# Kernel optimization log

Measured on AMD Instinct MI355X. Metric: run time of the kernel, lower is better.

Reference implementation:

```python
import jax, jax.numpy as jnp
import numpy as np


def setup_inputs() -> dict:
    key = jax.random.key(0)
    ks = jax.random.split(key, 5)
    B, C, H, W = 4, 256, 64, 64
    Cq = C // 8
    x = jax.random.normal(ks[0], (B, C, H, W), dtype=jnp.float32)
    Wq = jax.random.normal(ks[1], (Cq, C), dtype=jnp.float32) * (1.0 / np.sqrt(C))
    Wk = jax.random.normal(ks[2], (Cq, C), dtype=jnp.float32) * (1.0 / np.sqrt(C))
    Wv = jax.random.normal(ks[3], (C, C), dtype=jnp.float32) * (1.0 / np.sqrt(C))
    bq = jnp.zeros((Cq,), dtype=jnp.float32)
    bk = jnp.zeros((Cq,), dtype=jnp.float32)
    bv = jnp.zeros((C,), dtype=jnp.float32)
    gamma = jnp.ones((1,), dtype=jnp.float32)
    return {"x": x, "Wq": Wq, "bq": bq, "Wk": Wk, "bk": bk, "Wv": Wv, "bv": bv, "gamma": gamma}


def reference(x, Wq, bq, Wk, bk, Wv, bv, gamma):
    B, C, H, W = x.shape
    N = H * W
    xf = x.reshape(B, C, N)                      # (B, C, N)
    # 1x1 convs == per-pixel linear projections over channels
    q = jnp.einsum('dc,bcn->bdn', Wq, xf) + bq[None, :, None]   # (B, C/8, N)
    k = jnp.einsum('dc,bcn->bdn', Wk, xf) + bk[None, :, None]   # (B, C/8, N)
    v = jnp.einsum('dc,bcn->bdn', Wv, xf) + bv[None, :, None]   # (B, C,   N)
    # attention: note original has NO 1/sqrt(d) scaling
    scores = jnp.einsum('bdn,bdm->bnm', q, k)     # (B, N, N)
    attn = jax.nn.softmax(scores, axis=-1)
    out = jnp.einsum('bnm,bdm->bnd', attn, v)     # (B, N, C)
    out = out.transpose(0, 2, 1).reshape(B, C, H, W)
    return gamma * out + x
```

## Files before the change

kernel.cpp:

```cpp
#include <hip/hip_runtime.h>

#define BATCH 4
#define CH    256
#define DQ    32
#define NPIX  4096
#define LOG2E 1.44269504088896340736f

typedef unsigned short u16;
typedef unsigned int   u32;
typedef __attribute__((ext_vector_type(8))) short short8;
typedef __attribute__((ext_vector_type(16))) float f32x16;

__device__ __align__(16) u16 g_wbf[10 * 2 * 8192];
__device__ float g_bias[10 * 32];

__device__ __forceinline__ float b2f(u32 u) {
  union { u32 i; float f; } v; v.i = (u & 0xffffu) << 16; return v.f;
}
__device__ __forceinline__ u16 f2b(float f) {
  union { float f; u32 i; } v; v.f = f;
  u32 x = v.i; x += 0x7fffu + ((x >> 16) & 1u);
  return (u16)(x >> 16);
}
__device__ __forceinline__ float fexp2(float x) {
#if __has_builtin(__builtin_amdgcn_exp2f)
  return __builtin_amdgcn_exp2f(x);
#else
  return __expf(x * 0.69314718055994530942f);
#endif
}
__device__ __forceinline__ u32 cvtpk_bf16(float a, float b) {
  u32 r;
  asm("v_cvt_pk_bf16_f32 %0, %1, %2" : "=v"(r) : "v"(a), "v"(b));
  return r;
}

__device__ __forceinline__ void half_swap(u32 a0, u32 a1, u32 b0, u32 b1,
                                          int hl, uint4& o) {
#if __has_builtin(__builtin_amdgcn_permlane32_swap)
  const auto r0 = __builtin_amdgcn_permlane32_swap((int)a0, (int)b0, false, false);
  const auto r1 = __builtin_amdgcn_permlane32_swap((int)a1, (int)b1, false, false);
  o.x = (u32)r0[0]; o.y = (u32)r1[0]; o.z = (u32)r0[1]; o.w = (u32)r1[1];
#else
  const u32 s0 = hl ? a0 : b0;
  const u32 s1 = hl ? a1 : b1;
  const u32 r0 = (u32)__shfl_xor((int)s0, 32);
  const u32 r1 = (u32)__shfl_xor((int)s1, 32);
  o.x = hl ? r0 : a0; o.y = hl ? r1 : a1;
  o.z = hl ? b0 : r0; o.w = hl ? b1 : r1;
#endif
}

__global__ __launch_bounds__(256) void xprep(
    const float* __restrict__ x, u16* __restrict__ xt_hi, u16* __restrict__ xt_lo,
    const float* __restrict__ Wq, const float* __restrict__ bq,
    const float* __restrict__ Wk, const float* __restrict__ bk,
    const float* __restrict__ Wv, const float* __restrict__ bv)
{
  const int t = threadIdx.x;

  if (blockIdx.z == BATCH) {
    if (blockIdx.y != 0 || blockIdx.x >= 10) return;
    const int jt = blockIdx.x;
    const float* Wsrc; const float* bsrc; int jrow0; float scale = 1.f;
    if (jt == 0)      { Wsrc = Wq; bsrc = bq; jrow0 = 0; scale = LOG2E; }
    else if (jt == 1) { Wsrc = Wk; bsrc = bk; jrow0 = 0; }
    else              { Wsrc = Wv; bsrc = bv; jrow0 = (jt - 2) * 32; }
    u16* wdst = g_wbf + (size_t)jt * 16384;
    for (int i = 0; i < 32; ++i) {
      const int flat = i * 256 + t;
      const int j = flat >> 8, e = flat & 255;
      const float v = Wsrc[(size_t)(jrow0 + j) * CH + e] * scale;
      const u16 hi = f2b(v);
      const u16 lo = f2b(v - b2f(hi));
      const int idx = (((e >> 4) * 2 + ((e >> 3) & 1)) * 32 + j) * 8 + (e & 7);
      wdst[idx] = hi; wdst[8192 + idx] = lo;
    }
    if (t < 32) g_bias[jt * 32 + t] = bsrc[jrow0 + t] * scale;
    return;
  }

  const int nt = blockIdx.x, kb4 = blockIdx.y * 4, b = blockIdx.z;
  const int n0 = nt * 128, c0 = blockIdx.y * 64;
  __shared__ u32 xls[64][129];

  const int tn = t & 127, cp = t >> 7;
  for (int i = 0; i < 32; ++i) {
    const int c = cp + 2 * i;
    const float v = x[((size_t)b * CH + c0 + c) * NPIX + n0 + tn];
    const u16 h = f2b(v);
    const u16 l = f2b(v - b2f(h));
    xls[c][tn] = (u32)h | ((u32)l << 16);
  }
  __syncthreads();

  for (int rep = 0; rep < 4; ++rep) {
    const int id = t + 256 * rep;
    const int kkhl = id >> 7, n = id & 127;
    union { short8 s; uint4 u; } vh, vl;
    #pragma unroll
    for (int j = 0; j < 8; ++j) {
      const u32 p = xls[kkhl * 8 + j][n];
      vh.s[j] = (short)(p & 0xffffu);
      vl.s[j] = (short)(p >> 16);
    }
    const size_t o = ((((size_t)(b * 32 + nt) * 16 + kb4 + (kkhl >> 1)) * 2
                       + (kkhl & 1)) * 128 + n) * 8;
    *(uint4*)(xt_hi + o) = vh.u;
    *(uint4*)(xt_lo + o) = vl.u;
  }
}

__global__ __launch_bounds__(256, 4) void proj(
    const u16* __restrict__ xt_hi, const u16* __restrict__ xt_lo,
    u16* __restrict__ q_t, u16* __restrict__ k_t, u16* __restrict__ v_swz)
{
  const int L = blockIdx.x;
  const int xcd = L & 7, s = L >> 3;
  const int jt = s >> 4;
  const int pair = xcd * 16 + (s & 15);
  const int nt = pair >> 2, b = pair & 3;

  const int t = threadIdx.x;
  const int w = t >> 6, lane = t & 63, hl = lane >> 5, l31 = lane & 31;
  const int nb = w * 32 + l31, n = nt * 128 + nb;

  const u16* __restrict__ wb = g_wbf + (size_t)jt * 16384;
  const size_t xtile = (size_t)(b * 32 + nt) * 16 * 2 * 128 * 8;
  const u16* __restrict__ xh = xt_hi + xtile;
  const u16* __restrict__ xl = xt_lo + xtile;

  f32x16 acc1, acc2;
  #pragma unroll
  for (int r = 0; r < 16; ++r) { acc1[r] = 0.f; acc2[r] = 0.f; }

  #pragma unroll
  for (int kk = 0; kk < 16; ++kk) {
    const int aoff = ((kk * 2 + hl) * 32 + l31) * 8;
    const short8 wah = *(const short8*)(wb + aoff);
    const short8 wal = *(const short8*)(wb + 8192 + aoff);
    const int boff = ((kk * 2 + hl) * 128 + nb) * 8;
    const short8 xbh = *(const short8*)(xh + boff);
    const short8 xbl = *(const short8*)(xl + boff);
    acc1 = __builtin_amdgcn_mfma_f32_32x32x16_bf16(wah, xbh, acc1, 0, 0, 0);
    acc2 = __builtin_amdgcn_mfma_f32_32x32x16_bf16(wah, xbl, acc2, 0, 0, 0);
    acc2 = __builtin_amdgcn_mfma_f32_32x32x16_bf16(wal, xbh, acc2, 0, 0, 0);
  }

  f32x16 accv;
  #pragma unroll
  for (int r = 0; r < 16; ++r)
    accv[r] = acc1[r] + acc2[r]
            + g_bias[jt * 32 + (r & 3) + 8 * (r >> 2) + 4 * hl];

  if (jt <= 1) {
    u16* dst = (jt == 0) ? q_t : k_t;
    #pragma unroll
    for (int r2 = 0; r2 < 4; ++r2) {
      uint2 pk;
      pk.x = (u32)f2b(accv[4 * r2 + 0]) | ((u32)f2b(accv[4 * r2 + 1]) << 16);
      pk.y = (u32)f2b(accv[4 * r2 + 2]) | ((u32)f2b(accv[4 * r2 + 3]) << 16);
      *(uint2*)(dst + ((size_t)b * NPIX + n) * DQ + 4 * hl + 8 * r2) = pk;
    }
  } else {
    const int mc = nt * 4 + w;
    const int kc = (l31 >> 4) & 1, h3 = (l31 >> 3) & 1, j8 = l31 & 7;
    u16* dst = v_swz + (((((size_t)b * 128 + mc) * 8 + (jt - 2)) * 2 + kc) * 2 + h3) * 256 + j8;
    #pragma unroll
    for (int r = 0; r < 16; ++r) {
      const int c5 = (r & 3) + 8 * (r >> 2) + 4 * hl;
      dst[c5 * 8] = f2b(accv[r]);
    }
  }
}

__global__ __launch_bounds__(256, 2) void attn(
    const u16* __restrict__ q_t, const u16* __restrict__ k_t,
    const u16* __restrict__ v_swz, const float* __restrict__ x,
    const float* __restrict__ gamma, float* __restrict__ out)
{
  const int L = blockIdx.x;
  const int xcd = L & 7, slot = L >> 3;
  const int b = xcd >> 1;
  const int nt = slot * 2 + (xcd & 1);
  const int n0 = nt * 32;

  const int t = threadIdx.x;
  const int w = t >> 6, lane = t & 63, hl = lane >> 5, l31 = lane & 31;

  __shared__ float cbuf[8192];
  __shared__ float lbuf[4][64];

  short8 qf[2];
  #pragma unroll
  for (int kd = 0; kd < 2; ++kd)
    qf[kd] = *(const short8*)(q_t + ((size_t)b * NPIX + n0 + l31) * DQ + kd * 16 + hl * 8);

  f32x16 acc[8];
  #pragma unroll
  for (int ct = 0; ct < 8; ++ct)
    #pragma unroll
    for (int r = 0; r < 16; ++r) acc[ct][r] = 0.f;
  float lrun = 0.f;

  const u16* __restrict__ kb = k_t + (size_t)b * NPIX * DQ;

  f32x16 st;
  {
    const int mc0 = w * 32;
    const short8 kf0 = *(const short8*)(kb + (mc0 * 32 + l31) * DQ + hl * 8);
    const short8 kf1 = *(const short8*)(kb + (mc0 * 32 + l31) * DQ + 16 + hl * 8);
    #pragma unroll
    for (int r = 0; r < 16; ++r) st[r] = 0.f;
    st = __builtin_amdgcn_mfma_f32_32x32x16_bf16(kf0, qf[0], st, 0, 0, 0);
    st = __builtin_amdgcn_mfma_f32_32x32x16_bf16(kf1, qf[1], st, 0, 0, 0);
  }

  for (int cc = 0; cc < 32; ++cc) {
    const int mc = w * 32 + cc;

    u32 pk[4][2];
    #pragma unroll
    for (int g = 0; g < 4; ++g) {
      const float e0 = fexp2(st[4 * g + 0]);
      const float e1 = fexp2(st[4 * g + 1]);
      const float e2 = fexp2(st[4 * g + 2]);
      const float e3 = fexp2(st[4 * g + 3]);
      lrun += (e0 + e1) + (e2 + e3);
      pk[g][0] = cvtpk_bf16(e0, e1);
      pk[g][1] = cvtpk_bf16(e2, e3);
    }

    {
      const int mcn = w * 32 + ((cc < 31) ? cc + 1 : 31);
      const short8 kf0 = *(const short8*)(kb + (mcn * 32 + l31) * DQ + hl * 8);
      const short8 kf1 = *(const short8*)(kb + (mcn * 32 + l31) * DQ + 16 + hl * 8);
      #pragma unroll
      for (int r = 0; r < 16; ++r) st[r] = 0.f;
      st = __builtin_amdgcn_mfma_f32_32x32x16_bf16(kf0, qf[0], st, 0, 0, 0);
      st = __builtin_amdgcn_mfma_f32_32x32x16_bf16(kf1, qf[1], st, 0, 0, 0);
    }

    const size_t vbase = ((size_t)b * 128 + mc) * 8192;
    #pragma unroll
    for (int kc = 0; kc < 2; ++kc) {
      union { uint4 u; short8 s; } bu;
      half_swap(pk[2 * kc][0], pk[2 * kc][1], pk[2 * kc + 1][0], pk[2 * kc + 1][1], hl, bu.u);
      #pragma unroll
      for (int ct = 0; ct < 8; ++ct) {
        const short8 av = *(const short8*)(v_swz + vbase + (size_t)(((ct * 2 + kc) * 2 + hl) * 256) + l31 * 8);
        acc[ct] = __builtin_amdgcn_mfma_f32_32x32x16_bf16(av, bu.s, acc[ct], 0, 0, 0);
      }
    }
  }

  lbuf[w][lane] = lrun;
  __syncthreads();
  for (int src = 1; src < 4; ++src) {
    if (w == src) {
      #pragma unroll
      for (int ct = 0; ct < 8; ++ct)
        #pragma unroll
        for (int r = 0; r < 16; ++r)
          cbuf[(ct * 16 + r) * 64 + lane] = acc[ct][r];
    }
    __syncthreads();
    if (w == 0) {
      #pragma unroll
      for (int ct = 0; ct < 8; ++ct)
        #pragma unroll
        for (int r = 0; r < 16; ++r)
          acc[ct][r] += cbuf[(ct * 16 + r) * 64 + lane];
    }
    __syncthreads();
  }

  if (w == 0) {
    float l = (lbuf[0][lane] + lbuf[1][lane]) + (lbuf[2][lane] + lbuf[3][lane]);
    l += __shfl_xor(l, 32);
    const float linv = 1.0f / l;
    const float g = gamma[0];
    #pragma unroll
    for (int ct = 0; ct < 8; ++ct)
      #pragma unroll
      for (int r = 0; r < 16; ++r) {
        const int c = ct * 32 + (r & 3) + 8 * (r >> 2) + 4 * hl;
        const size_t idx = ((size_t)b * CH + c) * NPIX + n0 + l31;
        out[idx] = g * acc[ct][r] * linv + x[idx];
      }
  }
}

extern "C" void kernel_launch(void* const* d_in, const int* in_sizes, int n_in,
                              void* d_out, int out_size, void* d_ws, size_t ws_size,
                              hipStream_t stream) {
  const float* x  = (const float*)d_in[0];
  const float* Wq = (const float*)d_in[1];
  const float* bq = (const float*)d_in[2];
  const float* Wk = (const float*)d_in[3];
  const float* bk = (const float*)d_in[4];
  const float* Wv = (const float*)d_in[5];
  const float* bv = (const float*)d_in[6];
  const float* gm = (const float*)d_in[7];
  float* out = (float*)d_out;

  const size_t qk_elems = (size_t)BATCH * NPIX * DQ;
  const size_t v_elems  = (size_t)BATCH * NPIX * CH;
  const size_t need = (2 * qk_elems + v_elems) * sizeof(u16);
  if (ws_size < need) return;

  u16* q_t   = (u16*)d_ws;
  u16* k_t   = q_t + qk_elems;
  u16* v_swz = k_t + qk_elems;

  u16* xt_hi = (u16*)d_out;
  u16* xt_lo = xt_hi + (size_t)BATCH * NPIX * CH;

  xprep<<<dim3(NPIX / 128, CH / 64, BATCH + 1), 256, 0, stream>>>(
      x, xt_hi, xt_lo, Wq, bq, Wk, bk, Wv, bv);
  proj<<<dim3(32 * 10 * BATCH), 256, 0, stream>>>(xt_hi, xt_lo, q_t, k_t, v_swz);
  attn<<<dim3((NPIX / 32) * BATCH), 256, 0, stream>>>(q_t, k_t, v_swz, x, gm, out);
}
```

Measured before the change: 157.2 us.

## Prefetch K fragments two chunks ahead and parallelize the cross-wave reduction epilogue

```diff
diff --git a/kernel.cpp b/kernel.cpp
--- a/kernel.cpp
+++ b/kernel.cpp
@@ -206,18 +206,25 @@
   const u16* __restrict__ kb = k_t + (size_t)b * NPIX * DQ;
 
   f32x16 st;
+  short8 kfc0, kfc1;
   {
     const int mc0 = w * 32;
-    const short8 kf0 = *(const short8*)(kb + (mc0 * 32 + l31) * DQ + hl * 8);
-    const short8 kf1 = *(const short8*)(kb + (mc0 * 32 + l31) * DQ + 16 + hl * 8);
+    const short8 k00 = *(const short8*)(kb + (mc0 * 32 + l31) * DQ + hl * 8);
+    const short8 k01 = *(const short8*)(kb + (mc0 * 32 + l31) * DQ + 16 + hl * 8);
     #pragma unroll
     for (int r = 0; r < 16; ++r) st[r] = 0.f;
-    st = __builtin_amdgcn_mfma_f32_32x32x16_bf16(kf0, qf[0], st, 0, 0, 0);
-    st = __builtin_amdgcn_mfma_f32_32x32x16_bf16(kf1, qf[1], st, 0, 0, 0);
+    st = __builtin_amdgcn_mfma_f32_32x32x16_bf16(k00, qf[0], st, 0, 0, 0);
+    st = __builtin_amdgcn_mfma_f32_32x32x16_bf16(k01, qf[1], st, 0, 0, 0);
+    kfc0 = *(const short8*)(kb + ((mc0 + 1) * 32 + l31) * DQ + hl * 8);
+    kfc1 = *(const short8*)(kb + ((mc0 + 1) * 32 + l31) * DQ + 16 + hl * 8);
   }
 
   for (int cc = 0; cc < 32; ++cc) {
     const int mc = w * 32 + cc;
+
+    const int mcp = w * 32 + ((cc < 30) ? cc + 2 : 31);
+    const short8 kfn0 = *(const short8*)(kb + (mcp * 32 + l31) * DQ + hl * 8);
+    const short8 kfn1 = *(const short8*)(kb + (mcp * 32 + l31) * DQ + 16 + hl * 8);
 
     u32 pk[4][2];
     #pragma unroll
@@ -231,15 +238,10 @@
       pk[g][1] = cvtpk_bf16(e2, e3);
     }
 
-    {
-      const int mcn = w * 32 + ((cc < 31) ? cc + 1 : 31);
-      const short8 kf0 = *(const short8*)(kb + (mcn * 32 + l31) * DQ + hl * 8);
-      const short8 kf1 = *(const short8*)(kb + (mcn * 32 + l31) * DQ + 16 + hl * 8);
-      #pragma unroll
-      for (int r = 0; r < 16; ++r) st[r] = 0.f;
-      st = __builtin_amdgcn_mfma_f32_32x32x16_bf16(kf0, qf[0], st, 0, 0, 0);
-      st = __builtin_amdgcn_mfma_f32_32x32x16_bf16(kf1, qf[1], st, 0, 0, 0);
-    }
+    #pragma unroll
+    for (int r = 0; r < 16; ++r) st[r] = 0.f;
+    st = __builtin_amdgcn_mfma_f32_32x32x16_bf16(kfc0, qf[0], st, 0, 0, 0);
+    st = __builtin_amdgcn_mfma_f32_32x32x16_bf16(kfc1, qf[1], st, 0, 0, 0);
 
     const size_t vbase = ((size_t)b * 128 + mc) * 8192;
     #pragma unroll
@@ -252,42 +254,41 @@
         acc[ct] = __builtin_amdgcn_mfma_f32_32x32x16_bf16(av, bu.s, acc[ct], 0, 0, 0);
       }
     }
+
+    kfc0 = kfn0; kfc1 = kfn1;
   }
 
   lbuf[w][lane] = lrun;
   __syncthreads();
-  for (int src = 1; src < 4; ++src) {
+  for (int src = 0; src < 4; ++src) {
     if (w == src) {
       #pragma unroll
       for (int ct = 0; ct < 8; ++ct)
         #pragma unroll
-        for (int r = 0; r < 16; ++r)
-          cbuf[(ct * 16 + r) * 64 + lane] = acc[ct][r];
+        for (int r = 0; r < 16; ++r) {
+          const int idx = (ct * 16 + r) * 64 + lane;
+          if (src == 0) cbuf[idx] = acc[ct][r];
+          else          cbuf[idx] += acc[ct][r];
+        }
     }
     __syncthreads();
-    if (w == 0) {
-      #pragma unroll
-      for (int ct = 0; ct < 8; ++ct)
-        #pragma unroll
-        for (int r = 0; r < 16; ++r)
-          acc[ct][r] += cbuf[(ct * 16 + r) * 64 + lane];
-    }
-    __syncthreads();
-  }
-
-  if (w == 0) {
-    float l = (lbuf[0][lane] + lbuf[1][lane]) + (lbuf[2][lane] + lbuf[3][lane]);
-    l += __shfl_xor(l, 32);
-    const float linv = 1.0f / l;
-    const float g = gamma[0];
-    #pragma unroll
-    for (int ct = 0; ct < 8; ++ct)
-      #pragma unroll
-      for (int r = 0; r < 16; ++r) {
-        const int c = ct * 32 + (r & 3) + 8 * (r >> 2) + 4 * hl;
-        const size_t idx = ((size_t)b * CH + c) * NPIX + n0 + l31;
-        out[idx] = g * acc[ct][r] * linv + x[idx];
-      }
+  }
+
+  const int col = t & 31, chg = t >> 5;
+  float l = 0.f;
+  #pragma unroll
+  for (int gg = 0; gg < 4; ++gg)
+    l += lbuf[gg][col] + lbuf[gg][col + 32];
+  const float linv = 1.0f / l;
+  const float gmv = gamma[0];
+  #pragma unroll
+  for (int i = 0; i < 32; ++i) {
+    const int ch = chg * 32 + i;
+    const int ct = ch >> 5, c5 = ch & 31;
+    const int hl2 = (c5 >> 2) & 1, rl = c5 & 3, rh = c5 >> 3;
+    const float cb = cbuf[(ct * 16 + rh * 4 + rl) * 64 + hl2 * 32 + col];
+    const size_t oidx = ((size_t)b * CH + ch) * NPIX + n0 + col;
+    out[oidx] = gmv * cb * linv + x[oidx];
   }
 }
 
```

Result: slower. 179.9 us (+14.4%).
